# Kernel tuning notes

Measured on AMD Instinct MI355X. Metric: run time of the kernel, lower is better.

The kernel has to match this reference:

```python
import jax, jax.numpy as jnp
import numpy as np

B, S, D_IN, D = 8, 4096, 512, 256


def setup_inputs() -> dict:
    key = jax.random.key(0)
    ks = jax.random.split(key, 7)
    s_in = 1.0 / np.sqrt(D_IN)
    return {
        "x": jax.random.normal(ks[0], (B, S, D_IN), dtype=jnp.float32),
        "Wq": jax.random.normal(ks[1], (D_IN, D), dtype=jnp.float32) * s_in,
        "bq": jnp.zeros((D,), dtype=jnp.float32),
        "Wk": jax.random.normal(ks[2], (D_IN, D), dtype=jnp.float32) * s_in,
        "bk": jnp.zeros((D,), dtype=jnp.float32),
        "Wv": jax.random.normal(ks[3], (D_IN, D), dtype=jnp.float32) * s_in,
        "bv": jnp.zeros((D,), dtype=jnp.float32),
    }


def reference(x, Wq, bq, Wk, bk, Wv, bv):
    # Q/K/V projections (three Dense layers in the original)
    Q = jnp.einsum("bsd,de->bse", x, Wq) + bq  # [B,S,D]
    K = jnp.einsum("bsd,de->bse", x, Wk) + bk
    V = jnp.einsum("bsd,de->bse", x, Wv) + bv
    # scaled dot-product attention: softmax(QK^T / sqrt(d)) V
    scale = 1.0 / jnp.sqrt(jnp.asarray(Q.shape[-1], dtype=Q.dtype))
    scores = jnp.einsum("bqe,bke->bqk", Q, K) * scale  # [B,S,S]
    attn = jax.nn.softmax(scores, axis=-1)
    out = jnp.einsum("bqk,bke->bqe", attn, V)  # [B,S,D]
    return out
```

## Files before the change

kernel.cpp:

```cpp
#include <hip/hip_runtime.h>
#include <stdint.h>

#define B_   8
#define S_   4096
#define DIN  512
#define D_   256

typedef __attribute__((ext_vector_type(8))) short short8;
typedef __attribute__((ext_vector_type(4))) float floatx4;
typedef __attribute__((ext_vector_type(4))) short short4v;

__device__ __forceinline__ void gll16(const void* g, void* lds) {
  __builtin_amdgcn_global_load_lds(
      (const __attribute__((address_space(1))) void*)g,
      (__attribute__((address_space(3))) void*)lds, 16, 0, 0);
}
__device__ __forceinline__ short f2bf(float x) {
  union { float f; unsigned u; } c; c.f = x;
  unsigned r = (c.u + 0x7FFF + ((c.u >> 16) & 1)) >> 16;
  return (short)r;
}
__device__ __forceinline__ float bf2f(short v) {
  union { unsigned u; float f; } c; c.u = ((unsigned)(unsigned short)v) << 16;
  return c.f;
}

__global__ __launch_bounds__(256) void detect_kernel(
    const unsigned short* __restrict__ w, int* __restrict__ flag) {
  const int tid = threadIdx.x;
  float m = 0.f;
#pragma unroll
  for (int j = 0; j < 16; ++j) {
    float f = bf2f((short)w[tid * 16 + j]);
    m = fmaxf(m, fabsf(f));
  }
#pragma unroll
  for (int d = 1; d < 64; d <<= 1) m = fmaxf(m, __shfl_xor(m, d));
  __shared__ float red[4];
  if ((tid & 63) == 0) red[tid >> 6] = m;
  __syncthreads();
  if (tid == 0) {
    float mm = fmaxf(fmaxf(red[0], red[1]), fmaxf(red[2], red[3]));
    flag[0] = (mm > 1000.0f) ? 1 : 0;
  }
}

__global__ __launch_bounds__(256) void cvt_kernel(
    const void* __restrict__ src, short* __restrict__ dst, int n,
    const int* __restrict__ flag) {
  const int i = blockIdx.x * 256 + threadIdx.x;
  if (i * 4 >= n) return;
  if (*flag) {
    float4 v = ((const float4*)src)[i];
    short4v o;
    o[0] = f2bf(v.x); o[1] = f2bf(v.y); o[2] = f2bf(v.z); o[3] = f2bf(v.w);
    ((short4v*)dst)[i] = o;
  } else {
    ((short4v*)dst)[i] = ((const short4v*)src)[i];
  }
}

__global__ __launch_bounds__(256) void wt_kernel(
    const short* __restrict__ Wall, short* __restrict__ Wt) {
  __shared__ short tile[32][33];
  const int mat = blockIdx.z;
  const short* W = Wall + mat * (DIN * D_);
  const int n0 = blockIdx.x * 32, k0 = blockIdx.y * 32;
  const int tx = threadIdx.x & 31, ty = threadIdx.x >> 5;
#pragma unroll
  for (int i = 0; i < 4; ++i) {
    int k = ty + i * 8;
    tile[k][tx] = W[(k0 + k) * D_ + n0 + tx];
  }
  __syncthreads();
  short* o = Wt + mat * (D_ * DIN);
#pragma unroll
  for (int i = 0; i < 4; ++i) {
    int n = ty + i * 8;
    o[(n0 + n) * DIN + k0 + tx] = tile[tx][n];
  }
}

__global__ __launch_bounds__(256, 2) void qkv_kernel(
    const short* __restrict__ x, const short* __restrict__ Wt,
    const short* __restrict__ bb,
    short* __restrict__ Qg, short* __restrict__ Kg, short* __restrict__ Vtg) {
  __shared__ short As[2][512 * 8];
  __shared__ short Bs[2][512 * 8];
  const int tid = threadIdx.x;
  const int lane = tid & 63, w = tid >> 6;
  const int li = lane & 15, g = lane >> 4;
  const int mb = blockIdx.x;
  const int mat = blockIdx.y >> 1, nb = blockIdx.y & 1;
  const short* Ag = x + mb * 128 * DIN;
  const short* Bt = Wt + mat * (D_ * DIN) + nb * 128 * DIN;

  auto stage = [&](int buf, int k0) {
#pragma unroll
    for (int p = 0; p < 2; ++p) {
      int c = p * 256 + tid;
      int row = c >> 2, og = (c & 3) ^ (row & 3);
      gll16(Ag + row * DIN + k0 + og * 8, &As[buf][(p * 256 + w * 64) * 8]);
    }
#pragma unroll
    for (int p = 0; p < 2; ++p) {
      int c = p * 256 + tid;
      int row = c >> 2, og = (c & 3) ^ (row & 3);
      gll16(Bt + row * DIN + k0 + og * 8, &Bs[buf][(p * 256 + w * 64) * 8]);
    }
  };

  const int msub = (w & 1) * 64, nsub = (w >> 1) * 64;
  floatx4 acc[4][4];
#pragma unroll
  for (int i = 0; i < 4; ++i)
#pragma unroll
    for (int j = 0; j < 4; ++j) acc[i][j] = floatx4{0.f, 0.f, 0.f, 0.f};

  stage(0, 0);
  __syncthreads();
  for (int kt = 0; kt < 16; ++kt) {
    if (kt < 15) stage((kt + 1) & 1, (kt + 1) * 32);
    const int buf = kt & 1;
    short8 af[4], bfr[4];
#pragma unroll
    for (int mt = 0; mt < 4; ++mt) {
      int row = msub + mt * 16 + li;
      int og = g ^ (row & 3);
      af[mt] = *(const short8*)&As[buf][(row * 4 + og) * 8];
    }
#pragma unroll
    for (int nt = 0; nt < 4; ++nt) {
      int row = nsub + nt * 16 + li;
      int og = g ^ (row & 3);
      bfr[nt] = *(const short8*)&Bs[buf][(row * 4 + og) * 8];
    }
#pragma unroll
    for (int mt = 0; mt < 4; ++mt)
#pragma unroll
      for (int nt = 0; nt < 4; ++nt)
        acc[mt][nt] = __builtin_amdgcn_mfma_f32_16x16x32_bf16(
            af[mt], bfr[nt], acc[mt][nt], 0, 0, 0);
    __syncthreads();
  }

  const short* bias = bb + mat * 256;
  if (mat < 2) {
    short* O = (mat == 0) ? Qg : Kg;
#pragma unroll
    for (int nt = 0; nt < 4; ++nt) {
      float bv_ = bf2f(bias[nb * 128 + nsub + nt * 16 + li]);
#pragma unroll
      for (int mt = 0; mt < 4; ++mt)
#pragma unroll
        for (int r = 0; r < 4; ++r) {
          int m = mb * 128 + msub + mt * 16 + g * 4 + r;
          int n = nb * 128 + nsub + nt * 16 + li;
          O[m * D_ + n] = f2bf(acc[mt][nt][r] + bv_);
        }
    }
  } else {
#pragma unroll
    for (int nt = 0; nt < 4; ++nt) {
      float bv_ = bf2f(bias[nb * 128 + nsub + nt * 16 + li]);
#pragma unroll
      for (int mt = 0; mt < 4; ++mt) {
        int m0 = mb * 128 + msub + mt * 16 + g * 4;
        int batch = m0 >> 12, s = m0 & (S_ - 1);
        int n = nb * 128 + nsub + nt * 16 + li;
        short4v pk;
#pragma unroll
        for (int r = 0; r < 4; ++r) pk[r] = f2bf(acc[mt][nt][r] + bv_);
        *(short4v*)&Vtg[(batch * D_ + n) * S_ + s] = pk;
      }
    }
  }
}

__global__ __launch_bounds__(512, 2) void attn_kernel(
    const short* __restrict__ Qg, const short* __restrict__ Kg,
    const short* __restrict__ Vtg, void* __restrict__ outv,
    const int* __restrict__ flag) {
  __shared__ short Ks[2][2048 * 8];
  __shared__ short Vs[2][2048 * 8];
  __shared__ short Ps[8][16 * 72];
  const int tid = threadIdx.x, lane = tid & 63, w = tid >> 6;
  const int li = lane & 15, g = lane >> 4;
  const int bb = blockIdx.y, q0 = blockIdx.x * 128;
  const int qrow = q0 + w * 16;

  const short* Qb = Qg + (bb * S_ + qrow) * D_;
  const short* Kb = Kg + (size_t)bb * S_ * D_;
  const short* Vb = Vtg + (size_t)bb * D_ * S_;

  short8 qf[8];
#pragma unroll
  for (int o = 0; o < 8; ++o)
    qf[o] = *(const short8*)&Qb[li * D_ + o * 32 + g * 8];

  floatx4 oa[16];
#pragma unroll
  for (int i = 0; i < 16; ++i) oa[i] = floatx4{0.f, 0.f, 0.f, 0.f};
  float mst[4], lst[4];
#pragma unroll
  for (int r = 0; r < 4; ++r) { mst[r] = -1.0e30f; lst[r] = 0.f; }

  auto stage = [&](int t, int buf) {
    const int s0 = t * 64;
#pragma unroll
    for (int p = 0; p < 4; ++p) {
      int c = p * 512 + tid;
      int s = c >> 5, og = (c & 31) ^ (s & 31);
      gll16(&Kb[(s0 + s) * D_ + og * 8], &Ks[buf][(p * 512 + w * 64) * 8]);
    }
#pragma unroll
    for (int p = 0; p < 4; ++p) {
      int c = p * 512 + tid;
      int e = c >> 3, og = (c & 7) ^ (e & 7);
      gll16(&Vb[e * S_ + s0 + og * 8], &Vs[buf][(p * 512 + w * 64) * 8]);
    }
  };

  const float cs = 0.09016844005556f;
  stage(0, 0);
  __syncthreads();

  for (int t = 0; t < 64; ++t) {
    if (t < 63) stage(t + 1, (t + 1) & 1);
    const int buf = t & 1;

    floatx4 sc[4];
#pragma unroll
    for (int nt = 0; nt < 4; ++nt) sc[nt] = floatx4{0.f, 0.f, 0.f, 0.f};
#pragma unroll
    for (int nt = 0; nt < 4; ++nt) {
      const int sl = nt * 16 + li;
#pragma unroll
      for (int o = 0; o < 8; ++o) {
        int od = o * 4 + g;
        int chunk = sl * 32 + (od ^ (sl & 31));
        short8 kf = *(const short8*)&Ks[buf][chunk * 8];
        sc[nt] = __builtin_amdgcn_mfma_f32_16x16x32_bf16(qf[o], kf, sc[nt], 0, 0, 0);
      }
    }

    float rm[4];
#pragma unroll
    for (int r = 0; r < 4; ++r)
      rm[r] = fmaxf(fmaxf(sc[0][r], sc[1][r]), fmaxf(sc[2][r], sc[3][r]));
#pragma unroll
    for (int d = 1; d < 16; d <<= 1)
#pragma unroll
      for (int r = 0; r < 4; ++r)
        rm[r] = fmaxf(rm[r], __shfl_xor(rm[r], d));
    float al[4];
#pragma unroll
    for (int r = 0; r < 4; ++r) {
      float mn = fmaxf(mst[r], rm[r] * cs);
      al[r] = exp2f(mst[r] - mn);
      mst[r] = mn;
      lst[r] *= al[r];
    }
    float rs[4] = {0.f, 0.f, 0.f, 0.f};
#pragma unroll
    for (int nt = 0; nt < 4; ++nt)
#pragma unroll
      for (int r = 0; r < 4; ++r) {
        float p = exp2f(sc[nt][r] * cs - mst[r]);
        rs[r] += p;
        Ps[w][(g * 4 + r) * 72 + nt * 16 + li] = f2bf(p);
      }
#pragma unroll
    for (int d = 1; d < 16; d <<= 1)
#pragma unroll
      for (int r = 0; r < 4; ++r) rs[r] += __shfl_xor(rs[r], d);
#pragma unroll
    for (int r = 0; r < 4; ++r) lst[r] += rs[r];
#pragma unroll
    for (int i = 0; i < 16; ++i)
#pragma unroll
      for (int r = 0; r < 4; ++r) oa[i][r] *= al[r];

    __asm__ __volatile__("s_waitcnt lgkmcnt(0)" ::: "memory");

#pragma unroll
    for (int kb = 0; kb < 2; ++kb) {
      short8 pf = *(const short8*)&Ps[w][li * 72 + kb * 32 + g * 8];
#pragma unroll
      for (int n2 = 0; n2 < 16; ++n2) {
        int e = n2 * 16 + li, os = kb * 4 + g;
        int chunk = e * 8 + (os ^ (e & 7));
        short8 vf = *(const short8*)&Vs[buf][chunk * 8];
        oa[n2] = __builtin_amdgcn_mfma_f32_16x16x32_bf16(pf, vf, oa[n2], 0, 0, 0);
      }
    }
    __syncthreads();
  }

  const int f32o = *flag;
#pragma unroll
  for (int r = 0; r < 4; ++r) lst[r] = 1.0f / lst[r];
  if (f32o) {
    float* out = (float*)outv;
#pragma unroll
    for (int n2 = 0; n2 < 16; ++n2)
#pragma unroll
      for (int r = 0; r < 4; ++r) {
        int row = qrow + g * 4 + r, e = n2 * 16 + li;
        out[(bb * S_ + row) * D_ + e] = oa[n2][r] * lst[r];
      }
  } else {
    short* out = (short*)outv;
#pragma unroll
    for (int n2 = 0; n2 < 16; ++n2)
#pragma unroll
      for (int r = 0; r < 4; ++r) {
        int row = qrow + g * 4 + r, e = n2 * 16 + li;
        out[(bb * S_ + row) * D_ + e] = f2bf(oa[n2][r] * lst[r]);
      }
  }
}

extern "C" void kernel_launch(void* const* d_in, const int* in_sizes, int n_in,
                              void* d_out, int out_size, void* d_ws, size_t ws_size,
                              hipStream_t stream) {
  const void* x  = d_in[0];
  const void* Wq = d_in[1];
  const void* bq = d_in[2];
  const void* Wk = d_in[3];
  const void* bk = d_in[4];
  const void* Wv = d_in[5];
  const void* bv = d_in[6];
  char* ws = (char*)d_ws;
  int*   flag = (int*)(ws);
  short* bbuf = (short*)(ws + 256);
  short* wcv  = (short*)(ws + 4096);
  short* Wt   = (short*)(ws + (1u << 20));
  short* xb   = (short*)(ws + (2u << 20));
  short* Qw   = (short*)(ws + (34u << 20));
  short* Kw   = (short*)(ws + (50u << 20));
  short* Vtw  = (short*)(ws + (66u << 20));

  hipLaunchKernelGGL(detect_kernel, dim3(1), dim3(256), 0, stream,
                     (const unsigned short*)Wq, flag);
  hipLaunchKernelGGL(cvt_kernel, dim3(16384), dim3(256), 0, stream,
                     x, xb, B_ * S_ * DIN, flag);
  hipLaunchKernelGGL(cvt_kernel, dim3(128), dim3(256), 0, stream,
                     Wq, wcv + 0 * DIN * D_, DIN * D_, flag);
  hipLaunchKernelGGL(cvt_kernel, dim3(128), dim3(256), 0, stream,
                     Wk, wcv + 1 * DIN * D_, DIN * D_, flag);
  hipLaunchKernelGGL(cvt_kernel, dim3(128), dim3(256), 0, stream,
                     Wv, wcv + 2 * DIN * D_, DIN * D_, flag);
  hipLaunchKernelGGL(cvt_kernel, dim3(1), dim3(256), 0, stream,
                     bq, bbuf + 0 * D_, D_, flag);
  hipLaunchKernelGGL(cvt_kernel, dim3(1), dim3(256), 0, stream,
                     bk, bbuf + 1 * D_, D_, flag);
  hipLaunchKernelGGL(cvt_kernel, dim3(1), dim3(256), 0, stream,
                     bv, bbuf + 2 * D_, D_, flag);

  hipLaunchKernelGGL(wt_kernel, dim3(8, 16, 3), dim3(256), 0, stream, wcv, Wt);
  hipLaunchKernelGGL(qkv_kernel, dim3(256, 6), dim3(256), 0, stream,
                     xb, Wt, bbuf, Qw, Kw, Vtw);
  hipLaunchKernelGGL(attn_kernel, dim3(32, 8), dim3(512), 0, stream,
                     Qw, Kw, Vtw, d_out, flag);
}
```

Before: 391.1 us.

## Restructure attention kernel with 32-row warps, smaller KV tiles, lazy rescale; fuse weight conversion

```diff
diff --git a/kernel.cpp b/kernel.cpp
--- a/kernel.cpp
+++ b/kernel.cpp
@@ -1,4 +1,5 @@
 #include <hip/hip_runtime.h>
+#include <hip/hip_bf16.h>
 #include <stdint.h>
 
 #define B_   8
@@ -9,6 +10,7 @@
 typedef __attribute__((ext_vector_type(8))) short short8;
 typedef __attribute__((ext_vector_type(4))) float floatx4;
 typedef __attribute__((ext_vector_type(4))) short short4v;
+typedef __attribute__((ext_vector_type(2))) unsigned uint2v;
 
 __device__ __forceinline__ void gll16(const void* g, void* lds) {
   __builtin_amdgcn_global_load_lds(
@@ -23,6 +25,18 @@
 __device__ __forceinline__ float bf2f(short v) {
   union { unsigned u; float f; } c; c.u = ((unsigned)(unsigned short)v) << 16;
   return c.f;
+}
+__device__ __forceinline__ unsigned pk2bf(float a, float b) {
+  union { __hip_bfloat162 h; unsigned u; } c;
+  c.h = __float22bfloat162_rn(float2{a, b});
+  return c.u;
+}
+__device__ __forceinline__ float fexp2(float x) {
+#if __has_builtin(__builtin_amdgcn_exp2f)
+  return __builtin_amdgcn_exp2f(x);
+#else
+  return exp2f(x);
+#endif
 }
 
 __global__ __launch_bounds__(256) void detect_kernel(
@@ -60,25 +74,43 @@
   }
 }
 
-__global__ __launch_bounds__(256) void wt_kernel(
-    const short* __restrict__ Wall, short* __restrict__ Wt) {
-  __shared__ short tile[32][33];
+__global__ __launch_bounds__(256) void wtcvt_kernel(
+    const void* __restrict__ Wq, const void* __restrict__ Wk,
+    const void* __restrict__ Wv, short* __restrict__ Wt,
+    const int* __restrict__ flag) {
+  __shared__ float tile[32][33];
   const int mat = blockIdx.z;
-  const short* W = Wall + mat * (DIN * D_);
+  const void* W = (mat == 0) ? Wq : ((mat == 1) ? Wk : Wv);
   const int n0 = blockIdx.x * 32, k0 = blockIdx.y * 32;
   const int tx = threadIdx.x & 31, ty = threadIdx.x >> 5;
+  const bool f32 = (*flag != 0);
 #pragma unroll
   for (int i = 0; i < 4; ++i) {
     int k = ty + i * 8;
-    tile[k][tx] = W[(k0 + k) * D_ + n0 + tx];
+    float v = f32 ? ((const float*)W)[(k0 + k) * D_ + n0 + tx]
+                  : bf2f(((const short*)W)[(k0 + k) * D_ + n0 + tx]);
+    tile[k][tx] = v;
   }
   __syncthreads();
   short* o = Wt + mat * (D_ * DIN);
 #pragma unroll
   for (int i = 0; i < 4; ++i) {
     int n = ty + i * 8;
-    o[(n0 + n) * DIN + k0 + tx] = tile[tx][n];
-  }
+    o[(n0 + n) * DIN + k0 + tx] = f2bf(tile[tx][n]);
+  }
+}
+
+__global__ __launch_bounds__(256) void biascvt_kernel(
+    const void* __restrict__ bq, const void* __restrict__ bk,
+    const void* __restrict__ bv, short* __restrict__ bbuf,
+    const int* __restrict__ flag) {
+  const int tid = threadIdx.x;
+  const bool f32 = (*flag != 0);
+  const void* p[3] = {bq, bk, bv};
+#pragma unroll
+  for (int m = 0; m < 3; ++m)
+    bbuf[m * D_ + tid] = f32 ? f2bf(((const float*)p[m])[tid])
+                             : ((const short*)p[m])[tid];
 }
 
 __global__ __launch_bounds__(256, 2) void qkv_kernel(
@@ -177,47 +209,51 @@
   }
 }
 
-__global__ __launch_bounds__(512, 2) void attn_kernel(
+__global__ __launch_bounds__(256, 2) void attn_kernel(
     const short* __restrict__ Qg, const short* __restrict__ Kg,
     const short* __restrict__ Vtg, void* __restrict__ outv,
     const int* __restrict__ flag) {
-  __shared__ short Ks[2][2048 * 8];
-  __shared__ short Vs[2][2048 * 8];
-  __shared__ short Ps[8][16 * 72];
+  __shared__ short Ks[2][1024 * 8];
+  __shared__ short Vs[2][1024 * 8];
+  __shared__ short Ps[4][1024];
   const int tid = threadIdx.x, lane = tid & 63, w = tid >> 6;
   const int li = lane & 15, g = lane >> 4;
-  const int bb = blockIdx.y, q0 = blockIdx.x * 128;
-  const int qrow = q0 + w * 16;
+  const int id = blockIdx.x;
+  const int bb = id & 7, q0 = (id >> 3) * 128;
+  const int qrow = q0 + w * 32;
 
   const short* Qb = Qg + (bb * S_ + qrow) * D_;
   const short* Kb = Kg + (size_t)bb * S_ * D_;
   const short* Vb = Vtg + (size_t)bb * D_ * S_;
 
-  short8 qf[8];
-#pragma unroll
-  for (int o = 0; o < 8; ++o)
-    qf[o] = *(const short8*)&Qb[li * D_ + o * 32 + g * 8];
-
-  floatx4 oa[16];
-#pragma unroll
-  for (int i = 0; i < 16; ++i) oa[i] = floatx4{0.f, 0.f, 0.f, 0.f};
-  float mst[4], lst[4];
-#pragma unroll
-  for (int r = 0; r < 4; ++r) { mst[r] = -1.0e30f; lst[r] = 0.f; }
+  short8 qf[2][8];
+#pragma unroll
+  for (int qs = 0; qs < 2; ++qs)
+#pragma unroll
+    for (int o = 0; o < 8; ++o)
+      qf[qs][o] = *(const short8*)&Qb[(qs * 16 + li) * D_ + o * 32 + g * 8];
+
+  floatx4 oa[2][16];
+#pragma unroll
+  for (int qs = 0; qs < 2; ++qs)
+#pragma unroll
+    for (int i = 0; i < 16; ++i) oa[qs][i] = floatx4{0.f, 0.f, 0.f, 0.f};
+  float mst[2] = {-1.0e30f, -1.0e30f}, lst[2] = {0.f, 0.f};
 
   auto stage = [&](int t, int buf) {
-    const int s0 = t * 64;
+    const int s0 = t * 32;
 #pragma unroll
     for (int p = 0; p < 4; ++p) {
-      int c = p * 512 + tid;
-      int s = c >> 5, og = (c & 31) ^ (s & 31);
-      gll16(&Kb[(s0 + s) * D_ + og * 8], &Ks[buf][(p * 512 + w * 64) * 8]);
+      int c = p * 256 + tid;
+      int s = c >> 5, od = (c & 31) ^ s;
+      gll16(&Kb[(s0 + s) * D_ + od * 8], &Ks[buf][c * 8]);
     }
 #pragma unroll
     for (int p = 0; p < 4; ++p) {
-      int c = p * 512 + tid;
-      int e = c >> 3, og = (c & 7) ^ (e & 7);
-      gll16(&Vb[e * S_ + s0 + og * 8], &Vs[buf][(p * 512 + w * 64) * 8]);
+      int c = p * 256 + tid;
+      int row = c >> 3, k = (c & 7) ^ (row & 7);
+      int e = row * 2 + (k >> 2), so = k & 3;
+      gll16(&Vb[e * S_ + s0 + so * 8], &Vs[buf][c * 8]);
     }
   };
 
@@ -225,99 +261,135 @@
   stage(0, 0);
   __syncthreads();
 
-  for (int t = 0; t < 64; ++t) {
-    if (t < 63) stage(t + 1, (t + 1) & 1);
+  for (int t = 0; t < 128; ++t) {
+    if (t < 127) stage(t + 1, (t + 1) & 1);
     const int buf = t & 1;
 
-    floatx4 sc[4];
-#pragma unroll
-    for (int nt = 0; nt < 4; ++nt) sc[nt] = floatx4{0.f, 0.f, 0.f, 0.f};
-#pragma unroll
-    for (int nt = 0; nt < 4; ++nt) {
-      const int sl = nt * 16 + li;
-#pragma unroll
-      for (int o = 0; o < 8; ++o) {
-        int od = o * 4 + g;
-        int chunk = sl * 32 + (od ^ (sl & 31));
-        short8 kf = *(const short8*)&Ks[buf][chunk * 8];
-        sc[nt] = __builtin_amdgcn_mfma_f32_16x16x32_bf16(qf[o], kf, sc[nt], 0, 0, 0);
+    floatx4 sc[2][2];
+#pragma unroll
+    for (int qs = 0; qs < 2; ++qs)
+#pragma unroll
+      for (int nt = 0; nt < 2; ++nt) sc[qs][nt] = floatx4{0.f, 0.f, 0.f, 0.f};
+#pragma unroll
+    for (int o = 0; o < 8; ++o) {
+      short8 kf[2];
+#pragma unroll
+      for (int nt = 0; nt < 2; ++nt) {
+        int kc = nt * 16 + li, od = o * 4 + g;
+        kf[nt] = *(const short8*)&Ks[buf][(kc * 32 + (od ^ kc)) * 8];
       }
-    }
-
-    float rm[4];
-#pragma unroll
-    for (int r = 0; r < 4; ++r)
-      rm[r] = fmaxf(fmaxf(sc[0][r], sc[1][r]), fmaxf(sc[2][r], sc[3][r]));
-#pragma unroll
-    for (int d = 1; d < 16; d <<= 1)
-#pragma unroll
-      for (int r = 0; r < 4; ++r)
-        rm[r] = fmaxf(rm[r], __shfl_xor(rm[r], d));
-    float al[4];
-#pragma unroll
-    for (int r = 0; r < 4; ++r) {
-      float mn = fmaxf(mst[r], rm[r] * cs);
-      al[r] = exp2f(mst[r] - mn);
-      mst[r] = mn;
-      lst[r] *= al[r];
-    }
-    float rs[4] = {0.f, 0.f, 0.f, 0.f};
-#pragma unroll
-    for (int nt = 0; nt < 4; ++nt)
-#pragma unroll
-      for (int r = 0; r < 4; ++r) {
-        float p = exp2f(sc[nt][r] * cs - mst[r]);
-        rs[r] += p;
-        Ps[w][(g * 4 + r) * 72 + nt * 16 + li] = f2bf(p);
+#pragma unroll
+      for (int qs = 0; qs < 2; ++qs)
+#pragma unroll
+        for (int nt = 0; nt < 2; ++nt)
+          sc[qs][nt] = __builtin_amdgcn_mfma_f32_16x16x32_bf16(
+              kf[nt], qf[qs][o], sc[qs][nt], 0, 0, 0);
+    }
+
+    bool needs = false;
+    float al[2];
+#pragma unroll
+    for (int qs = 0; qs < 2; ++qs) {
+      float rm = sc[qs][0][0];
+#pragma unroll
+      for (int nt = 0; nt < 2; ++nt)
+#pragma unroll
+        for (int r = 0; r < 4; ++r) rm = fmaxf(rm, sc[qs][nt][r]);
+      rm = fmaxf(rm, __shfl_xor(rm, 16));
+      rm = fmaxf(rm, __shfl_xor(rm, 32));
+      float mn = fmaxf(mst[qs], rm * cs);
+      al[qs] = fexp2(mst[qs] - mn);
+      needs |= (mn > mst[qs]);
+      mst[qs] = mn;
+      lst[qs] *= al[qs];
+      float rs = 0.f;
+      float pv[2][4];
+#pragma unroll
+      for (int nt = 0; nt < 2; ++nt)
+#pragma unroll
+        for (int r = 0; r < 4; ++r) {
+          pv[nt][r] = fexp2(sc[qs][nt][r] * cs - mn);
+          rs += pv[nt][r];
+        }
+      rs += __shfl_xor(rs, 16);
+      rs += __shfl_xor(rs, 32);
+      lst[qs] += rs;
+      const int row = qs * 16 + li;
+#pragma unroll
+      for (int nt = 0; nt < 2; ++nt) {
+        uint2v u;
+        u[0] = pk2bf(pv[nt][0], pv[nt][1]);
+        u[1] = pk2bf(pv[nt][2], pv[nt][3]);
+        int c16 = nt * 2 + (g >> 1);
+        int addr = row * 32 + ((c16 ^ (row & 3)) * 8) + (g & 1) * 4;
+        *(uint2v*)&Ps[w][addr] = u;
       }
-#pragma unroll
-    for (int d = 1; d < 16; d <<= 1)
-#pragma unroll
-      for (int r = 0; r < 4; ++r) rs[r] += __shfl_xor(rs[r], d);
-#pragma unroll
-    for (int r = 0; r < 4; ++r) lst[r] += rs[r];
-#pragma unroll
-    for (int i = 0; i < 16; ++i)
-#pragma unroll
-      for (int r = 0; r < 4; ++r) oa[i][r] *= al[r];
+    }
+
+    if (__ballot(needs)) {
+#pragma unroll
+      for (int qs = 0; qs < 2; ++qs) {
+        float alr[4];
+#pragma unroll
+        for (int r = 0; r < 4; ++r) alr[r] = __shfl(al[qs], g * 4 + r, 16);
+#pragma unroll
+        for (int n2 = 0; n2 < 16; ++n2)
+#pragma unroll
+          for (int r = 0; r < 4; ++r) oa[qs][n2][r] *= alr[r];
+      }
+    }
 
     __asm__ __volatile__("s_waitcnt lgkmcnt(0)" ::: "memory");
 
-#pragma unroll
-    for (int kb = 0; kb < 2; ++kb) {
-      short8 pf = *(const short8*)&Ps[w][li * 72 + kb * 32 + g * 8];
-#pragma unroll
-      for (int n2 = 0; n2 < 16; ++n2) {
-        int e = n2 * 16 + li, os = kb * 4 + g;
-        int chunk = e * 8 + (os ^ (e & 7));
-        short8 vf = *(const short8*)&Vs[buf][chunk * 8];
-        oa[n2] = __builtin_amdgcn_mfma_f32_16x16x32_bf16(pf, vf, oa[n2], 0, 0, 0);
-      }
+    short8 pf[2];
+#pragma unroll
+    for (int qs = 0; qs < 2; ++qs) {
+      int row = qs * 16 + li;
+      pf[qs] = *(const short8*)&Ps[w][row * 32 + ((g ^ (row & 3)) * 8)];
+    }
+#pragma unroll
+    for (int n2 = 0; n2 < 16; ++n2) {
+      int e = n2 * 16 + li;
+      int row = e >> 1, k = (e & 1) * 4 + g;
+      short8 vf = *(const short8*)&Vs[buf][(row * 8 + (k ^ (row & 7))) * 8];
+#pragma unroll
+      for (int qs = 0; qs < 2; ++qs)
+        oa[qs][n2] = __builtin_amdgcn_mfma_f32_16x16x32_bf16(
+            pf[qs], vf, oa[qs][n2], 0, 0, 0);
     }
     __syncthreads();
   }
 
+  float lr[2][4];
+#pragma unroll
+  for (int qs = 0; qs < 2; ++qs) {
+    float inv = 1.0f / lst[qs];
+#pragma unroll
+    for (int r = 0; r < 4; ++r) lr[qs][r] = __shfl(inv, g * 4 + r, 16);
+  }
   const int f32o = *flag;
-#pragma unroll
-  for (int r = 0; r < 4; ++r) lst[r] = 1.0f / lst[r];
   if (f32o) {
     float* out = (float*)outv;
 #pragma unroll
-    for (int n2 = 0; n2 < 16; ++n2)
-#pragma unroll
-      for (int r = 0; r < 4; ++r) {
-        int row = qrow + g * 4 + r, e = n2 * 16 + li;
-        out[(bb * S_ + row) * D_ + e] = oa[n2][r] * lst[r];
-      }
+    for (int qs = 0; qs < 2; ++qs)
+#pragma unroll
+      for (int n2 = 0; n2 < 16; ++n2)
+#pragma unroll
+        for (int r = 0; r < 4; ++r) {
+          int row = qrow + qs * 16 + g * 4 + r, e = n2 * 16 + li;
+          out[(bb * S_ + row) * D_ + e] = oa[qs][n2][r] * lr[qs][r];
+        }
   } else {
     short* out = (short*)outv;
 #pragma unroll
-    for (int n2 = 0; n2 < 16; ++n2)
-#pragma unroll
-      for (int r = 0; r < 4; ++r) {
-        int row = qrow + g * 4 + r, e = n2 * 16 + li;
-        out[(bb * S_ + row) * D_ + e] = f2bf(oa[n2][r] * lst[r]);
-      }
+    for (int qs = 0; qs < 2; ++qs)
+#pragma unroll
+      for (int n2 = 0; n2 < 16; ++n2)
+#pragma unroll
+        for (int r = 0; r < 4; ++r) {
+          int row = qrow + qs * 16 + g * 4 + r, e = n2 * 16 + li;
+          out[(bb * S_ + row) * D_ + e] = f2bf(oa[qs][n2][r] * lr[qs][r]);
+        }
   }
 }
 
@@ -334,7 +406,6 @@
   char* ws = (char*)d_ws;
   int*   flag = (int*)(ws);
   short* bbuf = (short*)(ws + 256);
-  short* wcv  = (short*)(ws + 4096);
   short* Wt   = (short*)(ws + (1u << 20));
   short* xb   = (short*)(ws + (2u << 20));
   short* Qw   = (short*)(ws + (34u << 20));
@@ -345,22 +416,12 @@
                      (const unsigned short*)Wq, flag);
   hipLaunchKernelGGL(cvt_kernel, dim3(16384), dim3(256), 0, stream,
                      x, xb, B_ * S_ * DIN, flag);
-  hipLaunchKernelGGL(cvt_kernel, dim3(128), dim3(256), 0, stream,
-                     Wq, wcv + 0 * DIN * D_, DIN * D_, flag);
-  hipLaunchKernelGGL(cvt_kernel, dim3(128), dim3(256), 0, stream,
-                     Wk, wcv + 1 * DIN * D_, DIN * D_, flag);
-  hipLaunchKernelGGL(cvt_kernel, dim3(128), dim3(256), 0, stream,
-                     Wv, wcv + 2 * DIN * D_, DIN * D_, flag);
-  hipLaunchKernelGGL(cvt_kernel, dim3(1), dim3(256), 0, stream,
-                     bq, bbuf + 0 * D_, D_, flag);
-  hipLaunchKernelGGL(cvt_kernel, dim3(1), dim3(256), 0, stream,
-                     bk, bbuf + 1 * D_, D_, flag);
-  hipLaunchKernelGGL(cvt_kernel, dim3(1), dim3(256), 0, stream,
-                     bv, bbuf + 2 * D_, D_, flag);
-
-  hipLaunchKernelGGL(wt_kernel, dim3(8, 16, 3), dim3(256), 0, stream, wcv, Wt);
+  hipLaunchKernelGGL(wtcvt_kernel, dim3(8, 16, 3), dim3(256), 0, stream,
+                     Wq, Wk, Wv, Wt, flag);
+  hipLaunchKernelGGL(biascvt_kernel, dim3(1), dim3(256), 0, stream,
+                     bq, bk, bv, bbuf, flag);
   hipLaunchKernelGGL(qkv_kernel, dim3(256, 6), dim3(256), 0, stream,
                      xb, Wt, bbuf, Qw, Kw, Vtw);
-  hipLaunchKernelGGL(attn_kernel, dim3(32, 8), dim3(512), 0, stream,
+  hipLaunchKernelGGL(attn_kernel, dim3(256), dim3(256), 0, stream,
                      Qw, Kw, Vtw, d_out, flag);
 }
```

After: 725.6 us. 1.86x slower.
